# Optimization experiments

Hardware: AMD Instinct MI355X
Metric: run time of the kernel (lower is better)

The kernel has to match this reference:

```python
import math
import jax, jax.numpy as jnp
import numpy as np

DIM = 512
HEADS = 8
LS = 64  # local_size
SCALE = (DIM // HEADS) ** -0.5


def _normalize(x, eps=1e-12):
    # torch F.normalize(dim=-1): x / max(||x||, eps)
    n = jnp.linalg.norm(x, axis=-1, keepdims=True)
    return x / jnp.maximum(n, eps)


def setup_inputs() -> dict:
    key = jax.random.key(0)
    k0, k1, k2 = jax.random.split(key, 3)
    B, S, D = 8, 4096, DIM
    return {
        "x": jax.random.normal(k0, (B, S, D), jnp.float32),
        "W_qkv": jax.random.normal(k1, (D, 3 * D), jnp.float32) * 0.02,
        "b_qkv": jnp.zeros((3 * D,), jnp.float32),
        "W_proj": jax.random.normal(k2, (D, D), jnp.float32) * 0.02,
        "b_proj": jnp.zeros((D,), jnp.float32),
    }


def reference(x, W_qkv, b_qkv, W_proj, b_proj):
    B, S, D = x.shape
    H = HEADS
    d = D // H
    ls = LS
    nl = S // ls
    ntimes = int(math.log2(nl))

    # qkv projection -> [3, B, H, S, d]
    qkv = (x @ W_qkv + b_qkv).reshape(B, S, 3, H, d).transpose(2, 0, 3, 1, 4)
    q_pre = qkv[0].reshape(B * H, S, d).transpose(0, 2, 1)  # [BH, d, S]

    q_idx_last = jnp.broadcast_to(jnp.arange(S)[None, :], (B * H, S))

    # recursive content-based bipartition (unrolled: ntimes is static)
    for _ in range(ntimes):
        bh, dd, n = q_pre.shape
        q_avg = q_pre.reshape(bh, dd, 2, n // 2).mean(-1)        # [bh, d, 2]
        q_avg = _normalize(q_avg.transpose(0, 2, 1))             # [bh, 2, d]
        q_norm = _normalize(q_pre.transpose(0, 2, 1))            # [bh, n, d]
        # squared euclidean distance [bh, n, 2]
        sq = (jnp.sum(q_norm ** 2, -1)[:, :, None]
              + jnp.sum(q_avg ** 2, -1)[:, None, :]
              - 2.0 * jnp.einsum('bnd,bcd->bnc', q_norm, q_avg))
        q_ratio = (sq[:, :, 0] + 1.0) / (sq[:, :, 1] + 1.0)
        q_idx = jnp.argsort(q_ratio, axis=-1)                    # [bh, n]
        q_idx_last = jnp.take_along_axis(q_idx_last, q_idx, axis=-1).reshape(bh * 2, n // 2)
        q_pre = jnp.take_along_axis(q_pre, q_idx[:, None, :], axis=-1)
        # 'b d (c n) -> (b c) d n' with c=2
        q_pre = q_pre.reshape(bh, dd, 2, n // 2).transpose(0, 2, 1, 3).reshape(bh * 2, dd, n // 2)

    q_idx = q_idx_last.reshape(B, H, S)
    q_idx_rev = jnp.argsort(q_idx, axis=-1)

    # gather qkv along token dim with routed permutation
    qkv_pre = jnp.take_along_axis(qkv, q_idx[None, :, :, :, None], axis=3)  # [3,B,H,S,d]
    # 'qkv b h (nl ls) d -> qkv (b nl) h ls d'
    qkv_pre = qkv_pre.reshape(3, B, H, nl, ls, d).transpose(0, 1, 3, 2, 4, 5).reshape(3, B * nl, H, ls, d)
    q, k, v = qkv_pre[0], qkv_pre[1], qkv_pre[2]

    # windowed diff-softmax-mul attention (softmax over head dim d)
    attn = jax.nn.softmax((q - k) * SCALE, axis=-1)
    out = attn * v                                               # [(B nl), H, ls, d]

    # '(b nl) h ls d -> b h d (nl ls)'
    out = out.reshape(B, nl, H, ls, d).transpose(0, 2, 4, 1, 3).reshape(B, H, d, S)
    out = jnp.take_along_axis(out, q_idx_rev[:, :, None, :], axis=-1)
    res = out.reshape(B, D, S).transpose(0, 2, 1)                # [B, S, D]
    res = res @ W_proj + b_proj
    return x + res
```

## Files before the change

kernel.cpp:

```cpp
#include <hip/hip_runtime.h>
#include <hip/hip_bf16.h>

typedef __bf16 bf16;
typedef __attribute__((ext_vector_type(8))) __bf16 bf16x8;
typedef __attribute__((ext_vector_type(4))) __bf16 bf16x4;
typedef __attribute__((ext_vector_type(4))) float f32x4;

#define M_TOK 32768
#define D_    512
#define SCALE_ 0.125f

#define AS1 __attribute__((address_space(1)))
#define AS3 __attribute__((address_space(3)))

__global__ __launch_bounds__(256) void transpose_cvt_all(const float* __restrict__ Wqkv,
                                                         const float* __restrict__ Wproj,
                                                         bf16* __restrict__ Wq_t,
                                                         bf16* __restrict__ Wp_t) {
  __shared__ float tile[32][33];
  const int bx = blockIdx.x;
  const float* in;
  bf16* out;
  int N, n0;
  bool perm;
  if (bx < 48) { in = Wqkv;  out = Wq_t; N = 1536; n0 = bx * 32;        perm = true;  }
  else         { in = Wproj; out = Wp_t; N = 512;  n0 = (bx - 48) * 32; perm = false; }
  const int k0 = blockIdx.y * 32;
  const int tx = threadIdx.x, ty = threadIdx.y;
  for (int i = 0; i < 32; i += 8)
    tile[ty + i][tx] = in[(size_t)(k0 + ty + i) * N + n0 + tx];
  __syncthreads();
  for (int i = 0; i < 32; i += 8) {
    int n = n0 + ty + i;
    int np = n;
    if (perm) {
      int qkv = n >> 9, h = (n & 511) >> 6, c = n & 63;
      np = h * 192 + (c >> 4) * 48 + qkv * 16 + (c & 15);
    }
    out[(size_t)np * D_ + k0 + tx] = (bf16)tile[tx][ty + i];
  }
}

__global__ __launch_bounds__(512, 2) void fused_attn(const float* __restrict__ x,
                                                     const bf16* __restrict__ Wq_t,
                                                     const float* __restrict__ bqkv,
                                                     const bf16* __restrict__ Wp_t,
                                                     const float* __restrict__ bproj,
                                                     float* __restrict__ out) {
  __shared__ __align__(16) bf16 sX[64 * 512];
  __shared__ __align__(16) bf16 sY[2][512 * 32];
  __shared__ __align__(16) float sS[64 * 4];

  const int tid = threadIdx.x;
  const int w = tid >> 6, l = tid & 63;
  const int wrow = w >> 2, wcol = w & 3;
  const int m0 = blockIdx.x * 64;
  const int fr = l & 15, fkc = l >> 4, frs = fr & 7;
  const int rbase = fkc * 4;

#pragma unroll
  for (int q = 0; q < 8; ++q) {
    int u = tid + 512 * q;
    int row = u >> 6, slot = u & 63;
    int gch = (slot & 56) | ((slot & 7) ^ (row & 7));
    const float* gp = x + (size_t)(m0 + row) * D_ + gch * 8;
    f32x4 a = *(const f32x4*)gp;
    f32x4 b = *(const f32x4*)(gp + 4);
    bf16x8 v;
#pragma unroll
    for (int e = 0; e < 4; ++e) { v[e] = (bf16)a[e]; v[4 + e] = (bf16)b[e]; }
    *(bf16x8*)&sX[row * 512 + slot * 8] = v;
  }

  const int bsrow = tid >> 3;
  const int bgch  = (tid & 7) ^ (bsrow & 7);
  auto stageB = [&](int buf, int T) {
    const int hh = T >> 3, tt = T & 7;
#pragma unroll
    for (int q = 0; q < 3; ++q) {
      int row = 64 * q + bsrow;
      const bf16* gp = Wq_t + (size_t)(hh * 192 + row) * D_ + tt * 64 + bgch * 8;
      __builtin_amdgcn_global_load_lds((AS1 const void*)gp,
                                       (AS3 void*)&sY[buf][4096 * q + w * 512], 16, 0, 0);
    }
  };

  f32x4 acc[2][3];
  auto qkvK = [&](int buf, int tt, int kk) {
    const int cb = tt * 8 + kk * 4 + fkc;
    const int xslot = (cb & 56) | ((cb & 7) ^ frs);
    bf16x8 af[2], bfr[3];
#pragma unroll
    for (int i = 0; i < 2; ++i)
      af[i] = *(const bf16x8*)&sX[(wrow * 32 + i * 16 + fr) * 512 + xslot * 8];
    const int c2 = kk * 4 + fkc;
#pragma unroll
    for (int j = 0; j < 3; ++j)
      bfr[j] = *(const bf16x8*)&sY[buf][(wcol * 48 + j * 16 + fr) * 64 + (c2 ^ frs) * 8];
    __builtin_amdgcn_s_setprio(1);
#pragma unroll
    for (int i = 0; i < 2; ++i)
#pragma unroll
      for (int j = 0; j < 3; ++j)
        acc[i][j] = __builtin_amdgcn_mfma_f32_16x16x32_bf16(af[i], bfr[j], acc[i][j], 0, 0, 0);
    __builtin_amdgcn_s_setprio(0);
  };

  bf16x4 opk[8][2];

  stageB(0, 0);
  asm volatile("s_waitcnt lgkmcnt(0)" ::: "memory");

#pragma unroll
  for (int h = 0; h < 8; ++h) {
#pragma unroll
    for (int i = 0; i < 2; ++i)
#pragma unroll
      for (int j = 0; j < 3; ++j) {
        f32x4 z = {0.f, 0.f, 0.f, 0.f};
        acc[i][j] = z;
      }
#pragma unroll 2
    for (int t = 0; t < 8; ++t) {
      const int T = h * 8 + t;
      const int buf = t & 1;
      if (T < 63) {
        stageB(buf ^ 1, T + 1);
        asm volatile("s_waitcnt vmcnt(3)" ::: "memory");
      } else {
        asm volatile("s_waitcnt vmcnt(0)" ::: "memory");
      }
      __builtin_amdgcn_s_barrier();
      qkvK(buf, t, 0);
      qkvK(buf, t, 1);
      if (t == 7) {
        const int hcol = h * 64 + wcol * 16 + fr;
        const float bq = bqkv[hcol];
        const float bk = bqkv[512 + hcol];
        const float bv = bqkv[1024 + hcol];
        float ev[2][4];
#pragma unroll
        for (int i = 0; i < 2; ++i)
#pragma unroll
          for (int r = 0; r < 4; ++r) {
            float e = __expf((acc[i][0][r] + bq - acc[i][1][r] - bk) * SCALE_);
            ev[i][r] = e;
            float sm = e;
#pragma unroll
            for (int off = 1; off < 16; off <<= 1) sm += __shfl_xor(sm, off);
            if (fr == 0)
              sS[(wrow * 32 + i * 16 + rbase + r) * 4 + wcol] = sm;
          }
        asm volatile("s_waitcnt lgkmcnt(0)" ::: "memory");
        __builtin_amdgcn_s_barrier();
#pragma unroll
        for (int i = 0; i < 2; ++i) {
          bf16x4 p;
#pragma unroll
          for (int r = 0; r < 4; ++r) {
            f32x4 sv = *(const f32x4*)&sS[(wrow * 32 + i * 16 + rbase + r) * 4];
            float tot = (sv[0] + sv[1]) + (sv[2] + sv[3]);
            p[r] = (bf16)(ev[i][r] / tot * (acc[i][2][r] + bv));
          }
          opk[h][i] = p;
        }
      }
      __builtin_amdgcn_s_barrier();
    }
  }

  const int psrow = tid >> 2;
  const int pgch  = (tid & 3) ^ (psrow & 3);
  auto stageP = [&](int buf, int tk) {
#pragma unroll
    for (int q = 0; q < 4; ++q) {
      int row = 128 * q + psrow;
      const bf16* gp = Wp_t + (size_t)row * D_ + tk * 32 + pgch * 8;
      __builtin_amdgcn_global_load_lds((AS1 const void*)gp,
                                       (AS3 void*)&sY[buf][4096 * q + w * 512], 16, 0, 0);
    }
  };
  stageP(0, 0);
#pragma unroll
  for (int h = 0; h < 8; ++h)
#pragma unroll
    for (int i = 0; i < 2; ++i)
#pragma unroll
      for (int r = 0; r < 4; ++r) {
        int row = wrow * 32 + i * 16 + rbase + r;
        int col = h * 64 + wcol * 16 + fr;
        int c = col >> 3;
        int slot = (c & 56) | ((c & 7) ^ (row & 7));
        sX[row * 512 + slot * 8 + (col & 7)] = opk[h][i][r];
      }
  asm volatile("s_waitcnt lgkmcnt(0)" ::: "memory");
  __builtin_amdgcn_s_barrier();

  f32x4 pacc[2][8];
#pragma unroll
  for (int i = 0; i < 2; ++i)
#pragma unroll
    for (int j = 0; j < 8; ++j) {
      f32x4 z = {0.f, 0.f, 0.f, 0.f};
      pacc[i][j] = z;
    }

#pragma unroll 2
  for (int tk = 0; tk < 16; ++tk) {
    const int buf = tk & 1;
    if (tk < 15) {
      stageP(buf ^ 1, tk + 1);
      asm volatile("s_waitcnt vmcnt(4)" ::: "memory");
    } else {
      asm volatile("s_waitcnt vmcnt(0)" ::: "memory");
    }
    __builtin_amdgcn_s_barrier();
    const int cg = tk * 4 + fkc;
    const int xslot = (cg & 56) | ((cg & 7) ^ frs);
    bf16x8 paf[2], pbf[8];
#pragma unroll
    for (int i = 0; i < 2; ++i)
      paf[i] = *(const bf16x8*)&sX[(wrow * 32 + i * 16 + fr) * 512 + xslot * 8];
#pragma unroll
    for (int j = 0; j < 8; ++j) {
      int row = wcol * 128 + j * 16 + fr;
      pbf[j] = *(const bf16x8*)&sY[buf][row * 32 + (fkc ^ (fr & 3)) * 8];
    }
    __builtin_amdgcn_s_setprio(1);
#pragma unroll
    for (int i = 0; i < 2; ++i)
#pragma unroll
      for (int j = 0; j < 8; ++j)
        pacc[i][j] = __builtin_amdgcn_mfma_f32_16x16x32_bf16(paf[i], pbf[j], pacc[i][j], 0, 0, 0);
    __builtin_amdgcn_s_setprio(0);
    __builtin_amdgcn_s_barrier();
  }

#pragma unroll
  for (int j = 0; j < 8; ++j) {
    int n = wcol * 128 + j * 16 + fr;
    float bb = bproj[n];
#pragma unroll
    for (int i = 0; i < 2; ++i)
#pragma unroll
      for (int r = 0; r < 4; ++r) {
        int m = m0 + wrow * 32 + i * 16 + rbase + r;
        out[(size_t)m * D_ + n] = pacc[i][j][r] + bb + x[(size_t)m * D_ + n];
      }
  }
}

extern "C" void kernel_launch(void* const* d_in, const int* in_sizes, int n_in,
                              void* d_out, int out_size, void* d_ws, size_t ws_size,
                              hipStream_t stream) {
  const float* x     = (const float*)d_in[0];
  const float* Wqkv  = (const float*)d_in[1];
  const float* bqkv  = (const float*)d_in[2];
  const float* Wproj = (const float*)d_in[3];
  const float* bproj = (const float*)d_in[4];
  float* out = (float*)d_out;

  char* ws = (char*)d_ws;
  bf16* Wq_t = (bf16*)ws;
  bf16* Wp_t = (bf16*)(ws + (size_t)1536 * D_ * 2);

  transpose_cvt_all<<<dim3(64, 16), dim3(32, 8), 0, stream>>>(Wqkv, Wproj, Wq_t, Wp_t);

  fused_attn<<<dim3(M_TOK / 64), dim3(512), 0, stream>>>(x, Wq_t, bqkv, Wp_t, bproj, out);
}
```

Baseline: 281.2 us.

## Triple-buffer QKV weight staging, drop trailing barrier, fix proj LDS swizzle

Switches the QKV GEMM weight staging from double to triple buffering. Loads are issued two tiles ahead right after the barrier, which removes the second per-iteration barrier. It also changes the XOR swizzle for the projection weight tiles to use (row>>1)&3 to cut LDS bank conflicts, and fully unrolls both K loops. The shared buffer grows to 3x192x64 bf16, raising LDS per block, which may limit occupancy with launch_bounds(512,2).

New measurement: 324.1 us. +15.2%, slower.

```diff
diff --git a/kernel.cpp b/kernel.cpp
--- a/kernel.cpp
+++ b/kernel.cpp
@@ -48,7 +48,7 @@
                                                      const float* __restrict__ bproj,
                                                      float* __restrict__ out) {
   __shared__ __align__(16) bf16 sX[64 * 512];
-  __shared__ __align__(16) bf16 sY[2][512 * 32];
+  __shared__ __align__(16) bf16 sY[3 * 192 * 64];
   __shared__ __align__(16) float sS[64 * 4];
 
   const int tid = threadIdx.x;
@@ -81,7 +81,7 @@
       int row = 64 * q + bsrow;
       const bf16* gp = Wq_t + (size_t)(hh * 192 + row) * D_ + tt * 64 + bgch * 8;
       __builtin_amdgcn_global_load_lds((AS1 const void*)gp,
-                                       (AS3 void*)&sY[buf][4096 * q + w * 512], 16, 0, 0);
+                                       (AS3 void*)&sY[buf * 12288 + 4096 * q + w * 512], 16, 0, 0);
     }
   };
 
@@ -96,7 +96,7 @@
     const int c2 = kk * 4 + fkc;
 #pragma unroll
     for (int j = 0; j < 3; ++j)
-      bfr[j] = *(const bf16x8*)&sY[buf][(wcol * 48 + j * 16 + fr) * 64 + (c2 ^ frs) * 8];
+      bfr[j] = *(const bf16x8*)&sY[buf * 12288 + (wcol * 48 + j * 16 + fr) * 64 + (c2 ^ frs) * 8];
     __builtin_amdgcn_s_setprio(1);
 #pragma unroll
     for (int i = 0; i < 2; ++i)
@@ -109,7 +109,9 @@
   bf16x4 opk[8][2];
 
   stageB(0, 0);
+  stageB(1, 1);
   asm volatile("s_waitcnt lgkmcnt(0)" ::: "memory");
+  __builtin_amdgcn_s_barrier();
 
 #pragma unroll
   for (int h = 0; h < 8; ++h) {
@@ -120,17 +122,14 @@
         f32x4 z = {0.f, 0.f, 0.f, 0.f};
         acc[i][j] = z;
       }
-#pragma unroll 2
+#pragma unroll
     for (int t = 0; t < 8; ++t) {
       const int T = h * 8 + t;
-      const int buf = t & 1;
-      if (T < 63) {
-        stageB(buf ^ 1, T + 1);
-        asm volatile("s_waitcnt vmcnt(3)" ::: "memory");
-      } else {
-        asm volatile("s_waitcnt vmcnt(0)" ::: "memory");
-      }
+      const int buf = T % 3;
+      if (T < 63) asm volatile("s_waitcnt vmcnt(3)" ::: "memory");
+      else        asm volatile("s_waitcnt vmcnt(0)" ::: "memory");
       __builtin_amdgcn_s_barrier();
+      if (T < 62) stageB((T + 2) % 3, T + 2);
       qkvK(buf, t, 0);
       qkvK(buf, t, 1);
       if (t == 7) {
@@ -165,22 +164,21 @@
           opk[h][i] = p;
         }
       }
-      __builtin_amdgcn_s_barrier();
-    }
-  }
-
-  const int psrow = tid >> 2;
-  const int pgch  = (tid & 3) ^ (psrow & 3);
+    }
+  }
+
   auto stageP = [&](int buf, int tk) {
 #pragma unroll
     for (int q = 0; q < 4; ++q) {
-      int row = 128 * q + psrow;
-      const bf16* gp = Wp_t + (size_t)row * D_ + tk * 32 + pgch * 8;
+      int row = 128 * q + (tid >> 2);
+      int sch = (tid & 3) ^ ((tid >> 3) & 3);
+      const bf16* gp = Wp_t + (size_t)row * D_ + tk * 32 + sch * 8;
       __builtin_amdgcn_global_load_lds((AS1 const void*)gp,
-                                       (AS3 void*)&sY[buf][4096 * q + w * 512], 16, 0, 0);
+                                       (AS3 void*)&sY[buf * 16384 + 4096 * q + w * 512], 16, 0, 0);
     }
   };
   stageP(0, 0);
+
 #pragma unroll
   for (int h = 0; h < 8; ++h)
 #pragma unroll
@@ -205,7 +203,7 @@
       pacc[i][j] = z;
     }
 
-#pragma unroll 2
+#pragma unroll
   for (int tk = 0; tk < 16; ++tk) {
     const int buf = tk & 1;
     if (tk < 15) {
@@ -224,7 +222,7 @@
 #pragma unroll
     for (int j = 0; j < 8; ++j) {
       int row = wcol * 128 + j * 16 + fr;
-      pbf[j] = *(const bf16x8*)&sY[buf][row * 32 + (fkc ^ (fr & 3)) * 8];
+      pbf[j] = *(const bf16x8*)&sY[buf * 16384 + row * 32 + (fkc ^ ((fr >> 1) & 3)) * 8];
     }
     __builtin_amdgcn_s_setprio(1);
 #pragma unroll
```
